# Performance work log

Hardware: AMD Instinct MI355X
Metric: run time of the kernel (lower is better)

The kernel has to match this reference:

```python
import jax, jax.numpy as jnp
import numpy as np

BETA = 1.0  # inverse temperature (default of retrieve())
EPS = 1e-12  # matches torch F.normalize eps


def _l2_normalize(x):
    # torch.nn.functional.normalize(p=2, dim=-1): x / max(||x||, eps)
    n = jnp.sqrt(jnp.sum(x * x, axis=-1, keepdims=True))
    return x / jnp.maximum(n, EPS)


def setup_inputs() -> dict:
    key = jax.random.key(0)
    kq, kk = jax.random.split(key)
    N, K, D = 65536, 4096, 128
    queries = jax.random.normal(kq, (N, D), dtype=jnp.float32)
    # learnable memory keys, init_std = 0.02
    keys = jax.random.normal(kk, (K, D), dtype=jnp.float32) * 0.02
    return {"queries": queries, "keys": keys}


def reference(queries, keys):
    # normalize_keys=True, normalize_queries=True
    k_n = _l2_normalize(keys)
    q_n = _l2_normalize(queries)
    # values are TIED to the raw keys parameter (get_values returns self.keys,
    # un-normalized) — only the score-side keys are normalized.
    values = keys
    scores = BETA * jnp.einsum('nd,kd->nk', q_n, k_n)  # [N, K]
    attention = jax.nn.softmax(scores, axis=-1)
    retrieved = jnp.einsum('nk,kd->nd', attention, values)  # [N, D]
    return retrieved
```

## Files before the change

### kernel.cpp

```cpp
#include <hip/hip_runtime.h>
#include <hip/hip_bf16.h>
#include <stdint.h>


typedef __attribute__((ext_vector_type(8))) short bf16x8;
typedef __attribute__((ext_vector_type(16))) float f32x16;

#define MFMA32(a, b, c) __builtin_amdgcn_mfma_f32_32x32x16_bf16(a, b, c, 0, 0, 0)
#define ASYNC_CP16(gsrc, ldst)                                                  \
  __builtin_amdgcn_global_load_lds(                                             \
      (const __attribute__((address_space(1))) void*)(gsrc),                    \
      (__attribute__((address_space(3))) void*)(ldst), 16, 0, 0)

__device__ __forceinline__ unsigned pkbf(float lo, float hi) {
  union { __hip_bfloat162 h2; unsigned u; } v;
  v.h2 = __float22bfloat162_rn(float2{lo, hi});
  return v.u;
}

__global__ __launch_bounds__(256) void prep_k(const float* __restrict__ k,
                                              char* __restrict__ knf,
                                              char* __restrict__ vtf, int K) {
  __shared__ float sRaw[64 * 132];
  __shared__ float sScale[64];
  const int tid = threadIdx.x;
  const int kbase = blockIdx.x * 64;
  {
    const int key_loc = tid >> 2, dq = tid & 3;
    const float4* src = (const float4*)(k + (size_t)(kbase + key_loc) * 128 + dq * 32);
    float4 f[8];
    float ss = 0.f;
#pragma unroll
    for (int i = 0; i < 8; ++i) {
      f[i] = src[i];
      ss += f[i].x * f[i].x + f[i].y * f[i].y + f[i].z * f[i].z + f[i].w * f[i].w;
    }
    ss += __shfl_xor(ss, 1);
    ss += __shfl_xor(ss, 2);
    float4* dst = (float4*)(sRaw + key_loc * 132 + dq * 32);
#pragma unroll
    for (int i = 0; i < 8; ++i) dst[i] = f[i];
    if (dq == 0) sScale[key_loc] = ss > 0.f ? rsqrtf(ss) : 0.f;
  }
  __syncthreads();

#pragma unroll
  for (int r = 0; r < 4; ++r) {
    const int c = r * 256 + tid;
    const int t_loc = c >> 9, ds = (c >> 6) & 7, l = c & 63;
    const int h5 = l >> 5, c32 = l & 31;
    const int key_loc = t_loc * 32 + c32;
    const float sc = sScale[key_loc];
    const float* p = sRaw + key_loc * 132 + ds * 16 + h5 * 8;
    uint4 w;
    w.x = pkbf(p[0] * sc, p[1] * sc);
    w.y = pkbf(p[2] * sc, p[3] * sc);
    w.z = pkbf(p[4] * sc, p[5] * sc);
    w.w = pkbf(p[6] * sc, p[7] * sc);
    *(uint4*)(knf + ((size_t)blockIdx.x * 1024 + c) * 16) = w;
  }
#pragma unroll
  for (int r = 0; r < 4; ++r) {
    const int c = r * 256 + tid;
    const int s = c >> 8, db2 = (c >> 6) & 3, l = c & 63;
    const int h5 = l >> 5, c32 = l & 31;
    const int d = db2 * 32 + c32;
    const int kb = (s >> 1) * 32 + (s & 1) * 8 + h5 * 4;
    float f[8];
#pragma unroll
    for (int j = 0; j < 8; ++j)
      f[j] = sRaw[(kb + (j & 3) + (j >> 2) * 16) * 132 + d];
    uint4 w;
    w.x = pkbf(f[0], f[1]);
    w.y = pkbf(f[2], f[3]);
    w.z = pkbf(f[4], f[5]);
    w.w = pkbf(f[6], f[7]);
    *(uint4*)(vtf + ((size_t)blockIdx.x * 1024 + c) * 16) = w;
  }
}

__global__ __launch_bounds__(256, 2) void attn_main(
    const float* __restrict__ q, const char* __restrict__ knf,
    const char* __restrict__ vtf, float* __restrict__ out, int K) {
  __shared__ __align__(16) char sK[2][16384];
  const int tid = threadIdx.x;
  const int wave = tid >> 6, lane = tid & 63;
  const int h5 = lane >> 5, c32 = lane & 31;
  const int qrow0 = blockIdx.x * 128 + wave * 32;

  bf16x8 qf[8];
  {
    const float* qr = q + (size_t)(qrow0 + c32) * 128;
    float f[64];
    float ss = 0.f;
#pragma unroll
    for (int ds = 0; ds < 8; ++ds) {
      const float4 a = *(const float4*)(qr + ds * 16 + h5 * 8);
      const float4 b = *(const float4*)(qr + ds * 16 + h5 * 8 + 4);
      f[ds * 8 + 0] = a.x; f[ds * 8 + 1] = a.y; f[ds * 8 + 2] = a.z; f[ds * 8 + 3] = a.w;
      f[ds * 8 + 4] = b.x; f[ds * 8 + 5] = b.y; f[ds * 8 + 6] = b.z; f[ds * 8 + 7] = b.w;
    }
#pragma unroll
    for (int i = 0; i < 64; ++i) ss += f[i] * f[i];
    ss += __shfl_xor(ss, 32);
    const float sc = (ss > 0.f ? rsqrtf(ss) : 0.f) * 1.44269504f;
#pragma unroll
    for (int ds = 0; ds < 8; ++ds) {
      union { unsigned u[4]; bf16x8 v; } t;
#pragma unroll
      for (int p = 0; p < 4; ++p)
        t.u[p] = pkbf(f[ds * 8 + 2 * p] * sc, f[ds * 8 + 2 * p + 1] * sc);
      qf[ds] = t.v;
    }
  }

  f32x16 acc[4];
#pragma unroll
  for (int db2 = 0; db2 < 4; ++db2)
#pragma unroll
    for (int r = 0; r < 16; ++r) acc[db2][r] = 0.f;
  float den = 0.f;
  f32x16 Zf;
#pragma unroll
  for (int r = 0; r < 16; ++r) Zf[r] = 0.f;

  union pfu { unsigned u[4]; bf16x8 v; };
  pfu pf[4];
  f32x16 Sa[2], Sb[2];
  bf16x8 vcur[4];

  const int nIter = K >> 6;

  auto stage = [&](int it, int buf) {
#pragma unroll
    for (int i = 0; i < 4; ++i)
      ASYNC_CP16(knf + (size_t)it * 16384 + (wave * 4 + i) * 1024 + lane * 16,
                 sK[buf] + (wave * 4 + i) * 1024);
  };

  auto computeS = [&](int buf, f32x16* S) {
#pragma unroll
    for (int t = 0; t < 2; ++t) {
      f32x16 s;
#pragma unroll
      for (int ds = 0; ds < 8; ++ds) {
        const bf16x8 kf = *(const bf16x8*)(sK[buf] + (t * 8 + ds) * 1024 + lane * 16);
        s = MFMA32(kf, qf[ds], (ds == 0) ? Zf : s);
      }
      S[t] = s;
    }
  };

  auto doExp = [&](const f32x16* S) {
#pragma unroll
    for (int s = 0; s < 4; ++s) {
      const int t = s >> 1, w = s & 1;
      float e[8];
#pragma unroll
      for (int j = 0; j < 8; ++j) {
        const int rr = w * 4 + (j & 3) + (j >> 2) * 8;
        e[j] = __builtin_amdgcn_exp2f(S[t][rr]);
      }
      den += ((e[0] + e[1]) + (e[2] + e[3])) + ((e[4] + e[5]) + (e[6] + e[7]));
#pragma unroll
      for (int j2 = 0; j2 < 4; ++j2) pf[s].u[j2] = pkbf(e[2 * j2], e[2 * j2 + 1]);
    }
  };

  auto loadV0 = [&](int m) {
    const char* vbase = vtf + (size_t)m * 16384;
#pragma unroll
    for (int db2 = 0; db2 < 4; ++db2)
      vcur[db2] = *(const bf16x8*)(vbase + db2 * 1024 + lane * 16);
  };

  auto doPV = [&](int m) {
    const char* vbase = vtf + (size_t)m * 16384;
    bf16x8 vnxt[4];
#pragma unroll
    for (int s = 0; s < 4; ++s) {
      if (s < 3)
#pragma unroll
        for (int db2 = 0; db2 < 4; ++db2)
          vnxt[db2] = *(const bf16x8*)(vbase + ((s + 1) * 4 + db2) * 1024 + lane * 16);
#pragma unroll
      for (int db2 = 0; db2 < 4; ++db2)
        acc[db2] = MFMA32(vcur[db2], pf[s].v, acc[db2]);
      if (s < 3)
#pragma unroll
        for (int db2 = 0; db2 < 4; ++db2) vcur[db2] = vnxt[db2];
    }
  };

  stage(0, 0);
  __syncthreads();
  stage(1, 1);
  computeS(0, Sa);

  __syncthreads();
  stage(2, 0);
  loadV0(0);
  __builtin_amdgcn_s_setprio(1);
  computeS(1, Sb);
  doExp(Sa);
  doPV(0);
  __builtin_amdgcn_s_setprio(0);

  for (int itp = 2; itp < nIter; itp += 2) {
    __syncthreads();
    stage(itp + 1, 1);
    loadV0(itp - 1);
    __builtin_amdgcn_s_setprio(1);
    computeS(0, Sa);
    doExp(Sb);
    doPV(itp - 1);
    __builtin_amdgcn_s_setprio(0);

    __syncthreads();
    if (itp + 2 < nIter) stage(itp + 2, 0);
    loadV0(itp);
    __builtin_amdgcn_s_setprio(1);
    computeS(1, Sb);
    doExp(Sa);
    doPV(itp);
    __builtin_amdgcn_s_setprio(0);
  }

  loadV0(nIter - 1);
  doExp(Sb);
  doPV(nIter - 1);

  den += __shfl_xor(den, 32);
  const float rd = 1.0f / den;

  __syncthreads();
  float* wls = (float*)(&sK[0][0] + wave * 4096);
#pragma unroll
  for (int db2 = 0; db2 < 4; ++db2) {
#pragma unroll
    for (int qd = 0; qd < 4; ++qd) {
      float4 v;
      v.x = acc[db2][qd * 4 + 0] * rd;
      v.y = acc[db2][qd * 4 + 1] * rd;
      v.z = acc[db2][qd * 4 + 2] * rd;
      v.w = acc[db2][qd * 4 + 3] * rd;
      *(float4*)(wls + c32 * 32 + (((h5 + 2 * qd) ^ (c32 & 7)) << 2)) = v;
    }
#pragma unroll
    for (int p = 0; p < 4; ++p) {
      const int ql = p * 8 + (lane >> 3);
      const int x = lane & 7;
      const float4 v = *(const float4*)(wls + ql * 32 + ((x ^ (ql & 7)) << 2));
      *(float4*)(out + (size_t)(qrow0 + ql) * 128 + db2 * 32 + x * 4) = v;
    }
  }
}

extern "C" void kernel_launch(void* const* d_in, const int* in_sizes, int n_in,
                              void* d_out, int out_size, void* d_ws, size_t ws_size,
                              hipStream_t stream) {
  const float* q = (const float*)d_in[0];
  const float* k = (const float*)d_in[1];
  const int N = in_sizes[0] / 128;
  const int K = in_sizes[1] / 128;
  char* ws = (char*)d_ws;
  char* knf = ws;
  char* vtf = ws + (size_t)K * 256;
  float* out = (float*)d_out;

  prep_k<<<dim3(K / 64), dim3(256), 0, stream>>>(k, knf, vtf, K);
  attn_main<<<dim3(N / 128), dim3(256), 0, stream>>>(q, knf, vtf, out, K);
}
```

Baseline: 218.5 us.

## Stage V tiles through LDS with async copies instead of per-wave global loads

Each 64-key V tile is now loaded once per block into a double-buffered LDS region with async global-to-LDS copies and shared by all four waves. Previously every wave loaded the full V tile from global memory into registers. This cuts redundant global/L2 traffic and register pressure from the V prefetch. In exchange LDS use doubles to 64KB per block, which may limit how many blocks fit on a CU, and V reads now depend on the existing barrier schedule.

```diff
diff --git a/kernel.cpp b/kernel.cpp
--- a/kernel.cpp
+++ b/kernel.cpp
@@ -83,6 +83,7 @@
     const float* __restrict__ q, const char* __restrict__ knf,
     const char* __restrict__ vtf, float* __restrict__ out, int K) {
   __shared__ __align__(16) char sK[2][16384];
+  __shared__ __align__(16) char sV[2][16384];
   const int tid = threadIdx.x;
   const int wave = tid >> 6, lane = tid & 63;
   const int h5 = lane >> 5, c32 = lane & 31;
@@ -127,15 +128,20 @@
   union pfu { unsigned u[4]; bf16x8 v; };
   pfu pf[4];
   f32x16 Sa[2], Sb[2];
-  bf16x8 vcur[4];
 
   const int nIter = K >> 6;
 
-  auto stage = [&](int it, int buf) {
+  auto stageK = [&](int it, int buf) {
 #pragma unroll
     for (int i = 0; i < 4; ++i)
       ASYNC_CP16(knf + (size_t)it * 16384 + (wave * 4 + i) * 1024 + lane * 16,
                  sK[buf] + (wave * 4 + i) * 1024);
+  };
+  auto stageV = [&](int it, int buf) {
+#pragma unroll
+    for (int i = 0; i < 4; ++i)
+      ASYNC_CP16(vtf + (size_t)it * 16384 + (wave * 4 + i) * 1024 + lane * 16,
+                 sV[buf] + (wave * 4 + i) * 1024);
   };
 
   auto computeS = [&](int buf, f32x16* S) {
@@ -167,39 +173,30 @@
     }
   };
 
-  auto loadV0 = [&](int m) {
-    const char* vbase = vtf + (size_t)m * 16384;
-#pragma unroll
-    for (int db2 = 0; db2 < 4; ++db2)
-      vcur[db2] = *(const bf16x8*)(vbase + db2 * 1024 + lane * 16);
-  };
-
-  auto doPV = [&](int m) {
-    const char* vbase = vtf + (size_t)m * 16384;
-    bf16x8 vnxt[4];
+  auto doPV = [&](int buf) {
+    const char* vb = sV[buf] + lane * 16;
 #pragma unroll
     for (int s = 0; s < 4; ++s) {
-      if (s < 3)
-#pragma unroll
-        for (int db2 = 0; db2 < 4; ++db2)
-          vnxt[db2] = *(const bf16x8*)(vbase + ((s + 1) * 4 + db2) * 1024 + lane * 16);
-#pragma unroll
-      for (int db2 = 0; db2 < 4; ++db2)
-        acc[db2] = MFMA32(vcur[db2], pf[s].v, acc[db2]);
-      if (s < 3)
-#pragma unroll
-        for (int db2 = 0; db2 < 4; ++db2) vcur[db2] = vnxt[db2];
-    }
-  };
-
-  stage(0, 0);
-  __syncthreads();
-  stage(1, 1);
+      bf16x8 v0 = *(const bf16x8*)(vb + (s * 4 + 0) * 1024);
+      bf16x8 v1 = *(const bf16x8*)(vb + (s * 4 + 1) * 1024);
+      bf16x8 v2 = *(const bf16x8*)(vb + (s * 4 + 2) * 1024);
+      bf16x8 v3 = *(const bf16x8*)(vb + (s * 4 + 3) * 1024);
+      acc[0] = MFMA32(v0, pf[s].v, acc[0]);
+      acc[1] = MFMA32(v1, pf[s].v, acc[1]);
+      acc[2] = MFMA32(v2, pf[s].v, acc[2]);
+      acc[3] = MFMA32(v3, pf[s].v, acc[3]);
+    }
+  };
+
+  stageK(0, 0);
+  stageV(0, 0);
+  __syncthreads();
+  stageK(1, 1);
   computeS(0, Sa);
 
   __syncthreads();
-  stage(2, 0);
-  loadV0(0);
+  stageK(2, 0);
+  stageV(1, 1);
   __builtin_amdgcn_s_setprio(1);
   computeS(1, Sb);
   doExp(Sa);
@@ -208,27 +205,27 @@
 
   for (int itp = 2; itp < nIter; itp += 2) {
     __syncthreads();
-    stage(itp + 1, 1);
-    loadV0(itp - 1);
+    stageK(itp + 1, 1);
+    stageV(itp, 0);
     __builtin_amdgcn_s_setprio(1);
     computeS(0, Sa);
     doExp(Sb);
-    doPV(itp - 1);
+    doPV(1);
     __builtin_amdgcn_s_setprio(0);
 
     __syncthreads();
-    if (itp + 2 < nIter) stage(itp + 2, 0);
-    loadV0(itp);
+    if (itp + 2 < nIter) stageK(itp + 2, 0);
+    stageV(itp + 1, 1);
     __builtin_amdgcn_s_setprio(1);
     computeS(1, Sb);
     doExp(Sa);
-    doPV(itp);
+    doPV(0);
     __builtin_amdgcn_s_setprio(0);
   }
 
-  loadV0(nIter - 1);
+  __syncthreads();
   doExp(Sb);
-  doPV(nIter - 1);
+  doPV(1);
 
   den += __shfl_xor(den, 32);
   const float rd = 1.0f / den;
```

Result: faster. 202.3 us (-7.4%).
